# Kernel optimization log

Measured on AMD Instinct MI355X. Metric: run time of the kernel, lower is better.

## Reference

```python
import jax, jax.numpy as jnp
import numpy as np

NH, DK, W = 16, 64, 128        # n_heads, head_dim, sliding window
D = NH * DK                    # d_model = 1024
NEG = -1.0e9


def setup_inputs() -> dict:
    key = jax.random.key(0)
    k0, k1, k2, k3, k4 = jax.random.split(key, 5)
    L, B, T0 = 128, 8, 4096
    x_chunk = jax.random.normal(k0, (L, B, D), jnp.float32)
    K_cache = jax.random.normal(k1, (T0, B, NH, DK), jnp.float32)
    V_cache = jax.random.normal(k2, (T0, B, NH, DK), jnp.float32)
    s = 1.0 / np.sqrt(D)
    qkv_w = jax.random.normal(k3, (D, 3 * D), jnp.float32) * s
    qkv_b = jnp.zeros((3 * D,), jnp.float32)
    out_w = jax.random.normal(k4, (D, D), jnp.float32) * s
    out_b = jnp.zeros((D,), jnp.float32)
    return {"x_chunk": x_chunk, "K_cache": K_cache, "V_cache": V_cache,
            "qkv_w": qkv_w, "qkv_b": qkv_b, "out_w": out_w, "out_b": out_b}


def reference(x_chunk, K_cache, V_cache, qkv_w, qkv_b, out_w, out_b):
    L, B, Dm = x_chunk.shape
    qkv = (x_chunk @ qkv_w + qkv_b).reshape(L, B, 3, NH, DK)
    q, k, v = qkv[:, :, 0], qkv[:, :, 1], qkv[:, :, 2]
    K = jnp.concatenate([K_cache, k], axis=0)   # [T,B,nh,dk]
    V = jnp.concatenate([V_cache, v], axis=0)
    T = K.shape[0]
    idx = jnp.arange(T)
    # causal mask over global positions (rows = absolute key positions)
    mask = jnp.where(idx[None, :] > idx[:, None], NEG, 0.0)   # [T,T]
    if T > W:  # static shape -> Python if is fine under jit
        valid = jnp.zeros((T,), jnp.float32).at[-W:].set(1.0)
        mask = mask + (1.0 - valid[None, :]) * NEG
    # scores: [B,nh,L,T]
    logits = jnp.einsum('lbhd,tbhd->bhlt', q, K) / np.sqrt(DK)
    logits = logits + mask[-L:, :][None, None]
    weights = jax.nn.softmax(logits, axis=-1)
    o = jnp.einsum('bhlt,tbhd->lbhd', weights, V).reshape(L, B, Dm)
    y = o @ out_w + out_b
    return (y, K, V)
```

## Files before the change

### kernel.cpp

```cpp
#include <hip/hip_runtime.h>

#define L_CHUNK 128
#define BATCH   8
#define NHEADS  16
#define DKDIM   64
#define DMODEL  1024
#define T0CACHE 4096
#define TTOT    4224
#define ROWSTR  8192

#define N8PER   8388608u
#define CSPLIT  4194304u

typedef __attribute__((ext_vector_type(8))) __bf16 bf16x8;
typedef __attribute__((ext_vector_type(4))) float f32x4;
typedef __attribute__((ext_vector_type(8))) unsigned short us8;

__device__ __forceinline__ unsigned short f2bf(float f) {
    unsigned int u = __float_as_uint(f);
    u += 0x7fffu + ((u >> 16) & 1u);
    return (unsigned short)(u >> 16);
}

__device__ __forceinline__ void copy_slice(int cid, int ncopy,
        unsigned e0, unsigned e1,
        float4* __restrict__ Kd, const float4* __restrict__ Kc,
        float4* __restrict__ Vd, const float4* __restrict__ Vc) {
    const unsigned stride = (unsigned)ncopy * 256u;
    const unsigned base = e0 + (unsigned)cid * 256u + threadIdx.x;
    #pragma unroll 4
    for (unsigned e = base; e < e1; e += stride) Kd[e] = Kc[e];
    #pragma unroll 4
    for (unsigned e = base; e < e1; e += stride) Vd[e] = Vc[e];
}

template<int MODE, bool AF32, bool BF32>
__device__ __forceinline__ void gemm_body(
        int bx, int by,
        const void* __restrict__ Ap,
        const void* __restrict__ Bp,
        const float* __restrict__ bias,
        float* __restrict__ Cf, unsigned short* __restrict__ Cq,
        float* __restrict__ C1, float* __restrict__ C2,
        int K, int N) {
    __shared__ unsigned short Al[64][40];
    __shared__ unsigned short Bl[64][40];

    const int tid  = threadIdx.x;
    const int wave = tid >> 6;
    const int lane = tid & 63;
    const int m0 = by * 64;
    const int n0 = bx * 64;

    f32x4 zero = {0.f, 0.f, 0.f, 0.f};
    f32x4 acc[4];
    #pragma unroll
    for (int i = 0; i < 4; ++i) acc[i] = zero;

    const int ar = tid >> 2, ac = (tid & 3) * 8;
    const int bk = tid >> 3, bn = (tid & 7) * 8;
    const int rot = tid & 7;
    const int mrow = wave * 16 + (lane & 15);
    const int koff = (lane >> 4) * 8;

    float4 a0, a1, b0, b1;
    us8 a16, b16;

    auto LOAD = [&](int k0) {
        if constexpr (AF32) {
            const float* A = (const float*)Ap;
            a0 = *(const float4*)(A + (size_t)(m0 + ar) * K + (k0 + ac));
            a1 = *(const float4*)(A + (size_t)(m0 + ar) * K + (k0 + ac) + 4);
        } else {
            a16 = *(const us8*)((const unsigned short*)Ap + (size_t)(m0 + ar) * K + (k0 + ac));
        }
        if constexpr (BF32) {
            const float* B = (const float*)Bp;
            b0 = *(const float4*)(B + (size_t)(k0 + bk) * N + (n0 + bn));
            b1 = *(const float4*)(B + (size_t)(k0 + bk) * N + (n0 + bn) + 4);
        } else {
            b16 = *(const us8*)((const unsigned short*)Bp + (size_t)(k0 + bk) * N + (n0 + bn));
        }
    };
    auto STORE = [&]() {
        us8 av, bv;
        if constexpr (AF32) {
            av[0] = f2bf(a0.x); av[1] = f2bf(a0.y); av[2] = f2bf(a0.z); av[3] = f2bf(a0.w);
            av[4] = f2bf(a1.x); av[5] = f2bf(a1.y); av[6] = f2bf(a1.z); av[7] = f2bf(a1.w);
        } else av = a16;
        if constexpr (BF32) {
            bv[0] = f2bf(b0.x); bv[1] = f2bf(b0.y); bv[2] = f2bf(b0.z); bv[3] = f2bf(b0.w);
            bv[4] = f2bf(b1.x); bv[5] = f2bf(b1.y); bv[6] = f2bf(b1.z); bv[7] = f2bf(b1.w);
        } else bv = b16;
        *(us8*)(&Al[ar][ac]) = av;
        #pragma unroll
        for (int i = 0; i < 8; ++i) {
            int ii = (i + rot) & 7;
            Bl[bn + ii][bk] = bv[ii];
        }
    };
    auto COMPUTE = [&]() {
        bf16x8 af = __builtin_bit_cast(bf16x8, *(const us8*)(&Al[mrow][koff]));
        #pragma unroll
        for (int nt = 0; nt < 4; ++nt) {
            bf16x8 bf = __builtin_bit_cast(bf16x8,
                            *(const us8*)(&Bl[nt * 16 + (lane & 15)][koff]));
            acc[nt] = __builtin_amdgcn_mfma_f32_16x16x32_bf16(af, bf, acc[nt], 0, 0, 0);
        }
    };

    LOAD(0);
    STORE();
    __syncthreads();
    for (int k0 = 32; k0 < K; k0 += 32) {
        LOAD(k0);
        COMPUTE();
        __syncthreads();
        STORE();
        __syncthreads();
    }
    COMPUTE();

    const int colt  = lane & 15;
    const int rbase = (lane >> 4) * 4;
    #pragma unroll
    for (int nt = 0; nt < 4; ++nt) {
        int gcol = n0 + nt * 16 + colt;
        float bval = bias[gcol];
        #pragma unroll
        for (int r = 0; r < 4; ++r) {
            int grow = m0 + wave * 16 + rbase + r;
            float val = acc[nt][r] + bval;
            if (MODE == 0) {
                Cf[(size_t)grow * N + gcol] = val;
            } else {
                int s = gcol >> 10, w = gcol & 1023;
                int l = grow >> 3, b = grow & 7;
                size_t kvoff = (size_t)(T0CACHE + l) * ROWSTR + (size_t)b * DMODEL + w;
                if (s == 0)      Cq[(size_t)grow * DMODEL + w] = f2bf(val);
                else if (s == 1) C1[kvoff] = val;
                else             C2[kvoff] = val;
            }
        }
    }
}

__global__ __launch_bounds__(256) void qkv_gemm(
        const float* __restrict__ x,
        const float* __restrict__ qkv_w,
        const float* __restrict__ qkv_b,
        unsigned short* __restrict__ qb,
        float* __restrict__ Kout, float* __restrict__ Vout) {
    int gi = blockIdx.x;
    gemm_body<1, true, true>(gi % 48, gi / 48, x, qkv_w, qkv_b,
                             nullptr, qb, Kout, Vout, DMODEL, 3 * DMODEL);
}

__global__ __launch_bounds__(256) void attn_mfma(
        const unsigned short* __restrict__ qb,
        const float* __restrict__ Kout,
        const float* __restrict__ Vout,
        unsigned short* __restrict__ ob,
        const float4* __restrict__ Kc, const float4* __restrict__ Vc) {
    __shared__ unsigned short Kb[128][72];
    __shared__ unsigned short Vt[64][136];
    __shared__ unsigned short Pb[4][16][136];

    if (blockIdx.x >= 256) {
        copy_slice(blockIdx.x - 256, 2048, 0u, CSPLIT,
                   (float4*)Kout, Kc, (float4*)Vout, Vc);
        return;
    }

    const int tid  = threadIdx.x;
    const int wave = tid >> 6, lane = tid & 63;
    const int qh = blockIdx.x & 1, bh = blockIdx.x >> 1;
    const int b = bh >> 4, h = bh & 15;
    const int q0 = qh * 64;
    const size_t base = (size_t)T0CACHE * ROWSTR + (size_t)b * DMODEL + h * DKDIM;

    for (int e = tid; e < 2048; e += 256) {
        int j = e >> 4, d4 = (e & 15) * 4;
        float4 kv = *(const float4*)(Kout + base + (size_t)j * ROWSTR + d4);
        ushort4 u; u.x = f2bf(kv.x); u.y = f2bf(kv.y); u.z = f2bf(kv.z); u.w = f2bf(kv.w);
        *(ushort4*)&Kb[j][d4] = u;
        float4 vv = *(const float4*)(Vout + base + (size_t)j * ROWSTR + d4);
        Vt[d4 + 0][j] = f2bf(vv.x); Vt[d4 + 1][j] = f2bf(vv.y);
        Vt[d4 + 2][j] = f2bf(vv.z); Vt[d4 + 3][j] = f2bf(vv.w);
    }

    const int qrow = q0 + wave * 16 + (lane & 15);
    const size_t arow = (size_t)(qrow * 8 + b) * DMODEL + h * DKDIM;
    bf16x8 qa0 = __builtin_bit_cast(bf16x8, *(const us8*)(qb + arow + (lane >> 4) * 8));
    bf16x8 qa1 = __builtin_bit_cast(bf16x8, *(const us8*)(qb + arow + 32 + (lane >> 4) * 8));
    __syncthreads();

    f32x4 sacc[8];
    f32x4 zero = {0.f, 0.f, 0.f, 0.f};
    #pragma unroll
    for (int t = 0; t < 8; ++t) sacc[t] = zero;
    #pragma unroll
    for (int t = 0; t < 8; ++t) {
        bf16x8 k0 = __builtin_bit_cast(bf16x8,
                        *(const us8*)(&Kb[t * 16 + (lane & 15)][(lane >> 4) * 8]));
        bf16x8 k1 = __builtin_bit_cast(bf16x8,
                        *(const us8*)(&Kb[t * 16 + (lane & 15)][32 + (lane >> 4) * 8]));
        sacc[t] = __builtin_amdgcn_mfma_f32_16x16x32_bf16(qa0, k0, sacc[t], 0, 0, 0);
        sacc[t] = __builtin_amdgcn_mfma_f32_16x16x32_bf16(qa1, k1, sacc[t], 0, 0, 0);
    }

    const int col = lane & 15;
    float mrow[4], lsum[4], inv[4];
    #pragma unroll
    for (int r = 0; r < 4; ++r) mrow[r] = -3e38f;
    #pragma unroll
    for (int t = 0; t < 8; ++t) {
        #pragma unroll
        for (int r = 0; r < 4; ++r) {
            int key = t * 16 + col;
            int qi  = q0 + wave * 16 + (lane >> 4) * 4 + r;
            float v = sacc[t][r] * 0.125f;
            if (key > qi) v = -1e9f;
            sacc[t][r] = v;
            mrow[r] = fmaxf(mrow[r], v);
        }
    }
    #pragma unroll
    for (int r = 0; r < 4; ++r) {
        #pragma unroll
        for (int off = 1; off < 16; off <<= 1)
            mrow[r] = fmaxf(mrow[r], __shfl_xor(mrow[r], off, 64));
        lsum[r] = 0.f;
    }
    #pragma unroll
    for (int t = 0; t < 8; ++t) {
        #pragma unroll
        for (int r = 0; r < 4; ++r) {
            float p = __expf(sacc[t][r] - mrow[r]);
            lsum[r] += p;
            Pb[wave][(lane >> 4) * 4 + r][t * 16 + col] = f2bf(p);
        }
    }
    #pragma unroll
    for (int r = 0; r < 4; ++r) {
        #pragma unroll
        for (int off = 1; off < 16; off <<= 1)
            lsum[r] += __shfl_xor(lsum[r], off, 64);
        inv[r] = 1.f / lsum[r];
    }
    __syncthreads();

    bf16x8 pa[4];
    #pragma unroll
    for (int ks = 0; ks < 4; ++ks)
        pa[ks] = __builtin_bit_cast(bf16x8,
                     *(const us8*)(&Pb[wave][lane & 15][ks * 32 + (lane >> 4) * 8]));
    f32x4 oacc[4];
    #pragma unroll
    for (int n = 0; n < 4; ++n) oacc[n] = zero;
    #pragma unroll
    for (int n = 0; n < 4; ++n) {
        #pragma unroll
        for (int ks = 0; ks < 4; ++ks) {
            bf16x8 vb = __builtin_bit_cast(bf16x8,
                            *(const us8*)(&Vt[n * 16 + (lane & 15)][ks * 32 + (lane >> 4) * 8]));
            oacc[n] = __builtin_amdgcn_mfma_f32_16x16x32_bf16(pa[ks], vb, oacc[n], 0, 0, 0);
        }
    }

    #pragma unroll
    for (int n = 0; n < 4; ++n) {
        #pragma unroll
        for (int r = 0; r < 4; ++r) {
            int qi = q0 + wave * 16 + (lane >> 4) * 4 + r;
            int d  = n * 16 + col;
            ob[(size_t)(qi * 8 + b) * DMODEL + h * DKDIM + d] = f2bf(oacc[n][r] * inv[r]);
        }
    }
}

__global__ __launch_bounds__(256) void out_gemm(
        const unsigned short* __restrict__ ob,
        const float* __restrict__ out_w,
        const float* __restrict__ out_b, float* __restrict__ y,
        float* __restrict__ Kout, float* __restrict__ Vout,
        const float4* __restrict__ Kc, const float4* __restrict__ Vc) {
    const int g = blockIdx.x;
    if (g >= 256) {
        copy_slice(g - 256, 2048, CSPLIT, N8PER,
                   (float4*)Kout, Kc, (float4*)Vout, Vc);
        return;
    }
    gemm_body<0, false, true>(g & 15, g >> 4, ob, out_w, out_b,
                              y, nullptr, nullptr, nullptr, DMODEL, DMODEL);
}

extern "C" void kernel_launch(void* const* d_in, const int* in_sizes, int n_in,
                              void* d_out, int out_size, void* d_ws, size_t ws_size,
                              hipStream_t stream) {
    const float* x     = (const float*)d_in[0];
    const float* Kc    = (const float*)d_in[1];
    const float* Vc    = (const float*)d_in[2];
    const float* qkv_w = (const float*)d_in[3];
    const float* qkv_b = (const float*)d_in[4];
    const float* out_w = (const float*)d_in[5];
    const float* out_b = (const float*)d_in[6];

    float* y    = (float*)d_out;
    float* Kout = y + (size_t)L_CHUNK * BATCH * DMODEL;
    float* Vout = Kout + (size_t)TTOT * ROWSTR;

    char* ws = (char*)d_ws;
    unsigned short* qb = (unsigned short*)ws;
    unsigned short* ob = (unsigned short*)(ws + (size_t)(2 << 20));

    qkv_gemm<<<768, 256, 0, stream>>>(x, qkv_w, qkv_b, qb, Kout, Vout);

    attn_mfma<<<2304, 256, 0, stream>>>(qb, Kout, Vout, ob,
                                        (const float4*)Kc, (const float4*)Vc);

    out_gemm<<<2304, 256, 0, stream>>>(ob, out_w, out_b, y, Kout, Vout,
                                       (const float4*)Kc, (const float4*)Vc);
}
```

Baseline: 542.5 us.

## Pre-convert GEMM operands to bf16 in a prep kernel and rebalance cache copy

Adds a new first kernel that converts x, qkv_w and out_w to bf16 in workspace while other blocks copy the first slice of the KV cache. The two GEMMs then read bf16 operands directly, with no per-tile conversion. The cache copy is split three ways across the prep, attention and out-projection kernels so each launch overlaps a share of the bandwidth-bound copy. The attention kernel reuses its K shared buffer for P after an extra barrier, which lowers LDS use. The costs are an extra launch and a full extra pass over the weights each call.

New measurement: 531.8 us. -2.0%, faster.

```diff
diff --git a/kernel.cpp b/kernel.cpp
--- a/kernel.cpp
+++ b/kernel.cpp
@@ -10,7 +10,8 @@
 #define ROWSTR  8192
 
 #define N8PER   8388608u
-#define CSPLIT  4194304u
+#define SPLITA  3670016u
+#define SPLITB  6291456u
 
 typedef __attribute__((ext_vector_type(8))) __bf16 bf16x8;
 typedef __attribute__((ext_vector_type(4))) float f32x4;
@@ -28,17 +29,15 @@
         float4* __restrict__ Vd, const float4* __restrict__ Vc) {
     const unsigned stride = (unsigned)ncopy * 256u;
     const unsigned base = e0 + (unsigned)cid * 256u + threadIdx.x;
-    #pragma unroll 4
     for (unsigned e = base; e < e1; e += stride) Kd[e] = Kc[e];
-    #pragma unroll 4
     for (unsigned e = base; e < e1; e += stride) Vd[e] = Vc[e];
 }
 
-template<int MODE, bool AF32, bool BF32>
+template<int MODE>
 __device__ __forceinline__ void gemm_body(
         int bx, int by,
-        const void* __restrict__ Ap,
-        const void* __restrict__ Bp,
+        const unsigned short* __restrict__ A,
+        const unsigned short* __restrict__ B,
         const float* __restrict__ bias,
         float* __restrict__ Cf, unsigned short* __restrict__ Cq,
         float* __restrict__ C1, float* __restrict__ C2,
@@ -63,40 +62,18 @@
     const int mrow = wave * 16 + (lane & 15);
     const int koff = (lane >> 4) * 8;
 
-    float4 a0, a1, b0, b1;
     us8 a16, b16;
 
     auto LOAD = [&](int k0) {
-        if constexpr (AF32) {
-            const float* A = (const float*)Ap;
-            a0 = *(const float4*)(A + (size_t)(m0 + ar) * K + (k0 + ac));
-            a1 = *(const float4*)(A + (size_t)(m0 + ar) * K + (k0 + ac) + 4);
-        } else {
-            a16 = *(const us8*)((const unsigned short*)Ap + (size_t)(m0 + ar) * K + (k0 + ac));
-        }
-        if constexpr (BF32) {
-            const float* B = (const float*)Bp;
-            b0 = *(const float4*)(B + (size_t)(k0 + bk) * N + (n0 + bn));
-            b1 = *(const float4*)(B + (size_t)(k0 + bk) * N + (n0 + bn) + 4);
-        } else {
-            b16 = *(const us8*)((const unsigned short*)Bp + (size_t)(k0 + bk) * N + (n0 + bn));
-        }
+        a16 = *(const us8*)(A + (size_t)(m0 + ar) * K + (k0 + ac));
+        b16 = *(const us8*)(B + (size_t)(k0 + bk) * N + (n0 + bn));
     };
     auto STORE = [&]() {
-        us8 av, bv;
-        if constexpr (AF32) {
-            av[0] = f2bf(a0.x); av[1] = f2bf(a0.y); av[2] = f2bf(a0.z); av[3] = f2bf(a0.w);
-            av[4] = f2bf(a1.x); av[5] = f2bf(a1.y); av[6] = f2bf(a1.z); av[7] = f2bf(a1.w);
-        } else av = a16;
-        if constexpr (BF32) {
-            bv[0] = f2bf(b0.x); bv[1] = f2bf(b0.y); bv[2] = f2bf(b0.z); bv[3] = f2bf(b0.w);
-            bv[4] = f2bf(b1.x); bv[5] = f2bf(b1.y); bv[6] = f2bf(b1.z); bv[7] = f2bf(b1.w);
-        } else bv = b16;
-        *(us8*)(&Al[ar][ac]) = av;
+        *(us8*)(&Al[ar][ac]) = a16;
         #pragma unroll
         for (int i = 0; i < 8; ++i) {
             int ii = (i + rot) & 7;
-            Bl[bn + ii][bk] = bv[ii];
+            Bl[bn + ii][bk] = b16[ii];
         }
     };
     auto COMPUTE = [&]() {
@@ -145,15 +122,38 @@
     }
 }
 
+__global__ __launch_bounds__(256) void prep_and_copy(
+        const float* __restrict__ x, const float* __restrict__ qkv_w,
+        const float* __restrict__ out_w,
+        unsigned short* __restrict__ xb, unsigned short* __restrict__ wb,
+        unsigned short* __restrict__ owb,
+        float* __restrict__ Kout, float* __restrict__ Vout,
+        const float4* __restrict__ Kc, const float4* __restrict__ Vc) {
+    const int g = blockIdx.x;
+    if (g < 512) {
+        for (int idx = g * 256 + threadIdx.x; idx < 1310720; idx += 512 * 256) {
+            const float4* s4; ushort4* d4; int rel;
+            if (idx < 262144)        { s4 = (const float4*)x;     d4 = (ushort4*)xb;  rel = idx; }
+            else if (idx < 1048576)  { s4 = (const float4*)qkv_w; d4 = (ushort4*)wb;  rel = idx - 262144; }
+            else                     { s4 = (const float4*)out_w; d4 = (ushort4*)owb; rel = idx - 1048576; }
+            float4 v = s4[rel];
+            ushort4 o; o.x = f2bf(v.x); o.y = f2bf(v.y); o.z = f2bf(v.z); o.w = f2bf(v.w);
+            d4[rel] = o;
+        }
+    } else {
+        copy_slice(g - 512, 2048, 0u, SPLITA, (float4*)Kout, Kc, (float4*)Vout, Vc);
+    }
+}
+
 __global__ __launch_bounds__(256) void qkv_gemm(
-        const float* __restrict__ x,
-        const float* __restrict__ qkv_w,
+        const unsigned short* __restrict__ xb,
+        const unsigned short* __restrict__ wb,
         const float* __restrict__ qkv_b,
         unsigned short* __restrict__ qb,
         float* __restrict__ Kout, float* __restrict__ Vout) {
     int gi = blockIdx.x;
-    gemm_body<1, true, true>(gi % 48, gi / 48, x, qkv_w, qkv_b,
-                             nullptr, qb, Kout, Vout, DMODEL, 3 * DMODEL);
+    gemm_body<1>(gi % 48, gi / 48, xb, wb, qkv_b,
+                 nullptr, qb, Kout, Vout, DMODEL, 3 * DMODEL);
 }
 
 __global__ __launch_bounds__(256) void attn_mfma(
@@ -162,12 +162,11 @@
         const float* __restrict__ Vout,
         unsigned short* __restrict__ ob,
         const float4* __restrict__ Kc, const float4* __restrict__ Vc) {
-    __shared__ unsigned short Kb[128][72];
+    __shared__ unsigned short KPb[128][72];
     __shared__ unsigned short Vt[64][136];
-    __shared__ unsigned short Pb[4][16][136];
 
     if (blockIdx.x >= 256) {
-        copy_slice(blockIdx.x - 256, 2048, 0u, CSPLIT,
+        copy_slice(blockIdx.x - 256, 2048, SPLITA, SPLITB,
                    (float4*)Kout, Kc, (float4*)Vout, Vc);
         return;
     }
@@ -183,7 +182,7 @@
         int j = e >> 4, d4 = (e & 15) * 4;
         float4 kv = *(const float4*)(Kout + base + (size_t)j * ROWSTR + d4);
         ushort4 u; u.x = f2bf(kv.x); u.y = f2bf(kv.y); u.z = f2bf(kv.z); u.w = f2bf(kv.w);
-        *(ushort4*)&Kb[j][d4] = u;
+        *(ushort4*)&KPb[j][d4] = u;
         float4 vv = *(const float4*)(Vout + base + (size_t)j * ROWSTR + d4);
         Vt[d4 + 0][j] = f2bf(vv.x); Vt[d4 + 1][j] = f2bf(vv.y);
         Vt[d4 + 2][j] = f2bf(vv.z); Vt[d4 + 3][j] = f2bf(vv.w);
@@ -202,12 +201,15 @@
     #pragma unroll
     for (int t = 0; t < 8; ++t) {
         bf16x8 k0 = __builtin_bit_cast(bf16x8,
-                        *(const us8*)(&Kb[t * 16 + (lane & 15)][(lane >> 4) * 8]));
+                        *(const us8*)(&KPb[t * 16 + (lane & 15)][(lane >> 4) * 8]));
         bf16x8 k1 = __builtin_bit_cast(bf16x8,
-                        *(const us8*)(&Kb[t * 16 + (lane & 15)][32 + (lane >> 4) * 8]));
+                        *(const us8*)(&KPb[t * 16 + (lane & 15)][32 + (lane >> 4) * 8]));
         sacc[t] = __builtin_amdgcn_mfma_f32_16x16x32_bf16(qa0, k0, sacc[t], 0, 0, 0);
         sacc[t] = __builtin_amdgcn_mfma_f32_16x16x32_bf16(qa1, k1, sacc[t], 0, 0, 0);
     }
+    __syncthreads();
+
+    unsigned short* Pw = &KPb[0][0] + wave * 16 * 136;
 
     const int col = lane & 15;
     float mrow[4], lsum[4], inv[4];
@@ -238,7 +240,7 @@
         for (int r = 0; r < 4; ++r) {
             float p = __expf(sacc[t][r] - mrow[r]);
             lsum[r] += p;
-            Pb[wave][(lane >> 4) * 4 + r][t * 16 + col] = f2bf(p);
+            Pw[((lane >> 4) * 4 + r) * 136 + t * 16 + col] = f2bf(p);
         }
     }
     #pragma unroll
@@ -248,13 +250,12 @@
             lsum[r] += __shfl_xor(lsum[r], off, 64);
         inv[r] = 1.f / lsum[r];
     }
-    __syncthreads();
 
     bf16x8 pa[4];
     #pragma unroll
     for (int ks = 0; ks < 4; ++ks)
         pa[ks] = __builtin_bit_cast(bf16x8,
-                     *(const us8*)(&Pb[wave][lane & 15][ks * 32 + (lane >> 4) * 8]));
+                     *(const us8*)(Pw + (lane & 15) * 136 + ks * 32 + (lane >> 4) * 8));
     f32x4 oacc[4];
     #pragma unroll
     for (int n = 0; n < 4; ++n) oacc[n] = zero;
@@ -281,18 +282,18 @@
 
 __global__ __launch_bounds__(256) void out_gemm(
         const unsigned short* __restrict__ ob,
-        const float* __restrict__ out_w,
+        const unsigned short* __restrict__ owb,
         const float* __restrict__ out_b, float* __restrict__ y,
         float* __restrict__ Kout, float* __restrict__ Vout,
         const float4* __restrict__ Kc, const float4* __restrict__ Vc) {
     const int g = blockIdx.x;
     if (g >= 256) {
-        copy_slice(g - 256, 2048, CSPLIT, N8PER,
+        copy_slice(g - 256, 2048, SPLITB, N8PER,
                    (float4*)Kout, Kc, (float4*)Vout, Vc);
         return;
     }
-    gemm_body<0, false, true>(g & 15, g >> 4, ob, out_w, out_b,
-                              y, nullptr, nullptr, nullptr, DMODEL, DMODEL);
+    gemm_body<0>(g & 15, g >> 4, ob, owb, out_b,
+                 y, nullptr, nullptr, nullptr, DMODEL, DMODEL);
 }
 
 extern "C" void kernel_launch(void* const* d_in, const int* in_sizes, int n_in,
@@ -311,14 +312,21 @@
     float* Vout = Kout + (size_t)TTOT * ROWSTR;
 
     char* ws = (char*)d_ws;
-    unsigned short* qb = (unsigned short*)ws;
-    unsigned short* ob = (unsigned short*)(ws + (size_t)(2 << 20));
-
-    qkv_gemm<<<768, 256, 0, stream>>>(x, qkv_w, qkv_b, qb, Kout, Vout);
+    unsigned short* xb  = (unsigned short*)ws;
+    unsigned short* wb  = (unsigned short*)(ws + (size_t)(2  << 20));
+    unsigned short* owb = (unsigned short*)(ws + (size_t)(8  << 20));
+    unsigned short* qb  = (unsigned short*)(ws + (size_t)(10 << 20));
+    unsigned short* ob  = (unsigned short*)(ws + (size_t)(12 << 20));
+
+    prep_and_copy<<<2560, 256, 0, stream>>>(x, qkv_w, out_w, xb, wb, owb,
+                                            Kout, Vout,
+                                            (const float4*)Kc, (const float4*)Vc);
+
+    qkv_gemm<<<768, 256, 0, stream>>>(xb, wb, qkv_b, qb, Kout, Vout);
 
     attn_mfma<<<2304, 256, 0, stream>>>(qb, Kout, Vout, ob,
                                         (const float4*)Kc, (const float4*)Vc);
 
-    out_gemm<<<2304, 256, 0, stream>>>(ob, out_w, out_b, y, Kout, Vout,
+    out_gemm<<<2304, 256, 0, stream>>>(ob, owb, out_b, y, Kout, Vout,
                                        (const float4*)Kc, (const float4*)Vc);
 }
```
